# Optimization experiments

Measured on AMD Instinct MI355X. Metric: run time of the kernel, lower is better.

Reference implementation:

```python
import jax, jax.numpy as jnp
import numpy as np

NUM_BITS = 4
BLOCK = 64
OUT_F, IN_F = 4096, 4096
RANK = 16


def _uniform_table():
    # BlockQuantizer.create_uniform_map(symmetric=False, num_bits=4)
    return jnp.linspace(-1.0, 1.0, 2 ** NUM_BITS).astype(jnp.float32)


def _dequantize(qweight, weight_max):
    """Unpack 4-bit codes (2 per byte), lookup codebook, apply per-64 block scale.
    qweight: [OUT*IN/2, 1] int32 in [0,256); weight_max: [OUT*IN/64, 1] float32.
    Returns [OUT_F, IN_F] float32."""
    table = _uniform_table()
    q = qweight[:, 0]
    idx_lo = q & 15          # packed at shift 0
    idx_hi = (q >> 4) & 15   # packed at shift 4
    w = jnp.stack([table[idx_lo], table[idx_hi]], axis=-1)  # [N/2, 2]
    w = w.reshape(-1, BLOCK) * weight_max                   # per-block scale
    return w.reshape(OUT_F, IN_F)


def setup_inputs() -> dict:
    key = jax.random.key(0)
    k1, k2, k3, k4, k5, k6 = jax.random.split(key, 6)
    x = jax.random.normal(k1, (4, 2048, IN_F), dtype=jnp.float32)
    qweight = jax.random.randint(k2, (OUT_F * IN_F // 2, 1), 0, 256, dtype=jnp.int32)
    weight_max = jax.random.uniform(k3, (OUT_F * IN_F // BLOCK, 1), dtype=jnp.float32,
                                    minval=0.01, maxval=1.0)
    lora_A = jax.random.normal(k4, (RANK, IN_F), dtype=jnp.float32) * 0.02
    lora_B = jax.random.normal(k5, (OUT_F, RANK), dtype=jnp.float32) * 0.02
    bias = jax.random.normal(k6, (OUT_F,), dtype=jnp.float32) * 0.02
    return {"x": x, "qweight": qweight, "weight_max": weight_max,
            "lora_A": lora_A, "lora_B": lora_B, "bias": bias}


def reference(x, qweight, weight_max, lora_A, lora_B, bias):
    # Dequantize block-quantized base weight, then linear + LoRA correction.
    W = _dequantize(qweight, weight_max)                     # [out, in]
    y = jnp.einsum('bsi,oi->bso', x, W) + bias               # base linear
    a = jnp.einsum('bsi,ri->bsr', x, lora_A)                 # lora_A(x)
    y = y + jnp.einsum('bsr,or->bso', a, lora_B)             # + lora_B(.)
    return y
```

## Files before the change

### kernel.cpp

```cpp
#include <hip/hip_runtime.h>
#include <hip/hip_bf16.h>
#include <stdint.h>

typedef __bf16 bf16_t;
typedef bf16_t bf16x8 __attribute__((ext_vector_type(8)));
typedef float f32x4 __attribute__((ext_vector_type(4)));

#define IN_F 4096
#define OUT_F 4096
#define M_ROWS 8192
#define RANK 16

__global__ __launch_bounds__(256)
void dequant_lora_kernel(const int* __restrict__ qw, const float* __restrict__ wmax,
                         const float* __restrict__ lA, const float* __restrict__ lB,
                         bf16_t* __restrict__ Wp) {
  const int tid = blockIdx.x * 256 + threadIdx.x;
  const int f0 = tid * 8;
  const int o  = f0 >> 12;
  const int i0 = f0 & (IN_F - 1);
  const int4 q4 = *(const int4*)(qw + (f0 >> 1));
  const float scale = wmax[f0 >> 6];
  const float st = scale * (2.0f / 15.0f);

  float v[8];
  {
    const int q0 = q4.x, q1 = q4.y, q2 = q4.z, q3 = q4.w;
    v[0] = (float)(q0 & 15)        * st - scale;
    v[1] = (float)((q0 >> 4) & 15) * st - scale;
    v[2] = (float)(q1 & 15)        * st - scale;
    v[3] = (float)((q1 >> 4) & 15) * st - scale;
    v[4] = (float)(q2 & 15)        * st - scale;
    v[5] = (float)((q2 >> 4) & 15) * st - scale;
    v[6] = (float)(q3 & 15)        * st - scale;
    v[7] = (float)((q3 >> 4) & 15) * st - scale;
  }

  const float* Brow = lB + o * RANK;
#pragma unroll
  for (int r = 0; r < RANK; ++r) {
    const float br = Brow[r];
    const float4 a0 = *(const float4*)(lA + r * IN_F + i0);
    const float4 a1 = *(const float4*)(lA + r * IN_F + i0 + 4);
    v[0] += br * a0.x; v[1] += br * a0.y; v[2] += br * a0.z; v[3] += br * a0.w;
    v[4] += br * a1.x; v[5] += br * a1.y; v[6] += br * a1.z; v[7] += br * a1.w;
  }

  bf16x8 ov;
#pragma unroll
  for (int j = 0; j < 8; ++j) ov[j] = (bf16_t)v[j];
  *(bf16x8*)(Wp + (size_t)f0) = ov;
}

__global__ __launch_bounds__(256)
void f32_to_bf16_kernel(const float* __restrict__ x, bf16_t* __restrict__ xb) {
  const size_t tid = (size_t)blockIdx.x * 256 + threadIdx.x;
  const float4 a0 = *(const float4*)(x + tid * 8);
  const float4 a1 = *(const float4*)(x + tid * 8 + 4);
  bf16x8 o;
  o[0] = (bf16_t)a0.x; o[1] = (bf16_t)a0.y; o[2] = (bf16_t)a0.z; o[3] = (bf16_t)a0.w;
  o[4] = (bf16_t)a1.x; o[5] = (bf16_t)a1.y; o[6] = (bf16_t)a1.z; o[7] = (bf16_t)a1.w;
  *(bf16x8*)(xb + tid * 8) = o;
}

__device__ __forceinline__ void gld(const bf16_t* src, char* dst) {
  __builtin_amdgcn_global_load_lds((const __attribute__((address_space(1))) void*)src,
                                   (__attribute__((address_space(3))) void*)dst, 16, 0, 0);
}

#define BARRIER() __builtin_amdgcn_s_barrier()
#define SBAR()    __builtin_amdgcn_sched_barrier(0)
#define WAIT_VM(n) asm volatile("s_waitcnt vmcnt(" #n ")" ::: "memory")

#define LDA(buf, m, cb) (*(const bf16x8*)(ldsA + ((buf)*32768 + aRowB + (m)*2048 + (cb))))
#define LDB(buf, n, cb) (*(const bf16x8*)(ldsB + ((buf)*32768 + bRowB + (n)*2048 + (cb))))

#define STAGE_A4(kt, buf) do { \
  _Pragma("unroll") for (int g = 0; g < 4; ++g) \
    gld(Asrc + ((size_t)g*64*IN_F + (size_t)(kt)*64), ldsA + ((buf)*32768 + g*8192 + tid*16)); \
} while (0)
#define STAGE_B4(kt, buf) do { \
  _Pragma("unroll") for (int g = 0; g < 4; ++g) \
    gld(Bsrc + ((size_t)g*64*IN_F + (size_t)(kt)*64), ldsB + ((buf)*32768 + g*8192 + tid*16)); \
} while (0)

#define LOADA2(dst, m0, buf) do { \
  dst[0][0] = LDA(buf, m0,     cA0); dst[0][1] = LDA(buf, m0,     cA1); \
  dst[1][0] = LDA(buf, (m0)+1, cA0); dst[1][1] = LDA(buf, (m0)+1, cA1); \
} while (0)

#define PREFETCH12(buf, BFN) do { \
  LOADA2(aF0, 0, buf); \
  _Pragma("unroll") for (int n = 0; n < 4; ++n) { \
    BFN[n][0] = LDB(buf, n, cA0); BFN[n][1] = LDB(buf, n, cA1); } \
} while (0)

#define MFMA_Q(Q, AF, BF) do { \
  SBAR(); \
  __builtin_amdgcn_s_setprio(1); \
  _Pragma("unroll") for (int kh = 0; kh < 2; ++kh) \
  _Pragma("unroll") for (int mm = 0; mm < 2; ++mm) \
  _Pragma("unroll") for (int n = 0; n < 4; ++n) \
    acc[2*(Q)+mm][n] = __builtin_amdgcn_mfma_f32_16x16x32_bf16( \
        AF[mm][kh], BF[n][kh], acc[2*(Q)+mm][n], 0, 0, 0); \
  __builtin_amdgcn_s_setprio(0); \
} while (0)

#define TILE_BODY(CUR, BFC) do { \
  LOADA2(aF1, 2, CUR); MFMA_Q(0, aF0, BFC); \
  LOADA2(aF0, 4, CUR); MFMA_Q(1, aF1, BFC); \
  LOADA2(aF1, 6, CUR); MFMA_Q(2, aF0, BFC); \
  MFMA_Q(3, aF1, BFC); \
} while (0)

#define TILE_END(CUR, tv, BFN) do { \
  SBAR(); BARRIER(); \
  if ((tv) < 62) { STAGE_A4((tv) + 2, CUR); STAGE_B4((tv) + 2, CUR); \
                   SBAR(); WAIT_VM(8); } \
  else           { WAIT_VM(0); } \
  SBAR(); BARRIER(); SBAR(); \
  PREFETCH12((CUR) ^ 1, BFN); \
} while (0)

__global__ __launch_bounds__(512, 2)
void gemm_pipe_kernel(const bf16_t* __restrict__ Xb, const bf16_t* __restrict__ Wp,
                      const float* __restrict__ bias, float* __restrict__ C) {
  __shared__ __align__(16) bf16_t As[2 * 16384];
  __shared__ __align__(16) bf16_t Bs[2 * 16384];
  char* ldsA = (char*)As;
  char* ldsB = (char*)Bs;

  const int tid  = threadIdx.x;
  const int lane = tid & 63;
  const int wave = tid >> 6;
  const int wr = wave >> 2;
  const int wc = wave & 3;
  const int r16 = lane & 15;
  const int kg  = lane >> 4;

  const int bid = blockIdx.x;
  const int bm = bid >> 4;
  const int bn = bid & 15;

  const int sr = tid >> 3;
  const int sc = ((tid & 7) ^ (sr & 7)) << 3;
  const bf16_t* Asrc = Xb + (size_t)(bm * 256 + sr) * IN_F + sc;
  const bf16_t* Bsrc = Wp + (size_t)(bn * 256 + sr) * IN_F + sc;

  const int aRowB = (wr * 128 + r16) * 128;
  const int bRowB = (wc * 64 + r16) * 128;
  const int cA0 = (kg * 16) ^ ((r16 & 7) << 4);
  const int cA1 = cA0 ^ 64;

  f32x4 acc[8][4] = {};
  bf16x8 aF0[2][2], aF1[2][2], bFe[4][2], bFo[4][2];

  STAGE_A4(0, 0); STAGE_B4(0, 0);
  STAGE_A4(1, 1); STAGE_B4(1, 1);
  WAIT_VM(8);
  BARRIER(); SBAR();
  PREFETCH12(0, bFe);

  for (int tt = 0; tt < 62; tt += 2) {
    TILE_BODY(0, bFe); TILE_END(0, tt,     bFo);
    TILE_BODY(1, bFo); TILE_END(1, tt + 1, bFe);
  }
  TILE_BODY(0, bFe); TILE_END(0, 62, bFo);
  TILE_BODY(1, bFo);

#pragma unroll
  for (int n = 0; n < 4; ++n) {
    const int col = bn * 256 + wc * 64 + n * 16 + r16;
    const float bv = bias[col];
#pragma unroll
    for (int m = 0; m < 8; ++m) {
      const int row0 = bm * 256 + wr * 128 + m * 16 + kg * 4;
#pragma unroll
      for (int r = 0; r < 4; ++r)
        C[(size_t)(row0 + r) * OUT_F + col] = acc[m][n][r] + bv;
    }
  }
}

extern "C" void kernel_launch(void* const* d_in, const int* in_sizes, int n_in,
                              void* d_out, int out_size, void* d_ws, size_t ws_size,
                              hipStream_t stream) {
  const float* x  = (const float*)d_in[0];
  const int*   qw = (const int*)d_in[1];
  const float* wm = (const float*)d_in[2];
  const float* lA = (const float*)d_in[3];
  const float* lB = (const float*)d_in[4];
  const float* bs = (const float*)d_in[5];
  float* out = (float*)d_out;

  bf16_t* Wp = (bf16_t*)d_ws;
  bf16_t* Xb = (bf16_t*)((char*)d_ws + (size_t)OUT_F * IN_F * 2);

  dequant_lora_kernel<<<OUT_F * IN_F / 8 / 256, 256, 0, stream>>>(qw, wm, lA, lB, Wp);
  f32_to_bf16_kernel<<<M_ROWS * IN_F / 8 / 256, 256, 0, stream>>>(x, Xb);
  gemm_pipe_kernel<<<(M_ROWS / 256) * (OUT_F / 256), 512, 0, stream>>>(Xb, Wp, bs, out);
}
```

Before: 344.0 us.

## Load GEMM A operand directly from global memory into registers, skip LDS staging

The GEMM kernel stops staging the X (A) tile through LDS. Each wave now loads its A fragments straight from global memory into registers a quarter-tile ahead, and only the weight (B) tile still goes through LDS double-buffering, which halves LDS footprint and barrier-coupled traffic. The dequant kernel is also remapped so each block covers an 8-row by 256-column tile, which gives better LoRA A reuse. The risk is that direct global A loads repeat across the four column waves and expose memory latency, which relies on L1/L2 hits and the prefetch distance.

```diff
diff --git a/kernel.cpp b/kernel.cpp
--- a/kernel.cpp
+++ b/kernel.cpp
@@ -15,10 +15,14 @@
 void dequant_lora_kernel(const int* __restrict__ qw, const float* __restrict__ wmax,
                          const float* __restrict__ lA, const float* __restrict__ lB,
                          bf16_t* __restrict__ Wp) {
-  const int tid = blockIdx.x * 256 + threadIdx.x;
-  const int f0 = tid * 8;
-  const int o  = f0 >> 12;
-  const int i0 = f0 & (IN_F - 1);
+  const int bid = blockIdx.x;
+  const int bo = bid >> 4;
+  const int bi = bid & 15;
+  const int t  = threadIdx.x;
+  const int o  = bo * 8 + (t >> 5);
+  const int i0 = bi * 256 + (t & 31) * 8;
+  const int f0 = o * IN_F + i0;
+
   const int4 q4 = *(const int4*)(qw + (f0 >> 1));
   const float scale = wmax[f0 >> 6];
   const float st = scale * (2.0f / 15.0f);
@@ -72,27 +76,26 @@
 #define SBAR()    __builtin_amdgcn_sched_barrier(0)
 #define WAIT_VM(n) asm volatile("s_waitcnt vmcnt(" #n ")" ::: "memory")
 
-#define LDA(buf, m, cb) (*(const bf16x8*)(ldsA + ((buf)*32768 + aRowB + (m)*2048 + (cb))))
-#define LDB(buf, n, cb) (*(const bf16x8*)(ldsB + ((buf)*32768 + bRowB + (n)*2048 + (cb))))
-
-#define STAGE_A4(kt, buf) do { \
+#define STAGE_B(kt, buf) do { \
   _Pragma("unroll") for (int g = 0; g < 4; ++g) \
-    gld(Asrc + ((size_t)g*64*IN_F + (size_t)(kt)*64), ldsA + ((buf)*32768 + g*8192 + tid*16)); \
-} while (0)
-#define STAGE_B4(kt, buf) do { \
-  _Pragma("unroll") for (int g = 0; g < 4; ++g) \
-    gld(Bsrc + ((size_t)g*64*IN_F + (size_t)(kt)*64), ldsB + ((buf)*32768 + g*8192 + tid*16)); \
-} while (0)
-
-#define LOADA2(dst, m0, buf) do { \
-  dst[0][0] = LDA(buf, m0,     cA0); dst[0][1] = LDA(buf, m0,     cA1); \
-  dst[1][0] = LDA(buf, (m0)+1, cA0); dst[1][1] = LDA(buf, (m0)+1, cA1); \
-} while (0)
-
-#define PREFETCH12(buf, BFN) do { \
-  LOADA2(aF0, 0, buf); \
+    gld(Bsrc + (size_t)g * 64 * IN_F + (size_t)(kt) * 64, \
+        ldsB + (buf) * 32768 + g * 8192 + tid * 16); \
+} while (0)
+
+#define LDB(buf, n, kh) \
+  (*(const bf16x8*)(ldsB + (buf)*32768 + bRowB + (n)*2048 + cB##kh))
+
+#define PREF_B(buf, BFN) do { \
   _Pragma("unroll") for (int n = 0; n < 4; ++n) { \
-    BFN[n][0] = LDB(buf, n, cA0); BFN[n][1] = LDB(buf, n, cA1); } \
+    BFN[n][0] = LDB(buf, n, 0); BFN[n][1] = LDB(buf, n, 1); } \
+} while (0)
+
+#define PREF_A(dst, Q, tv) do { \
+  const bf16_t* _ap = Abase + (size_t)((Q) * 32) * IN_F + (tv) * 64; \
+  dst[0][0] = *(const bf16x8*)(_ap); \
+  dst[0][1] = *(const bf16x8*)(_ap + 32); \
+  dst[1][0] = *(const bf16x8*)(_ap + (size_t)16 * IN_F); \
+  dst[1][1] = *(const bf16x8*)(_ap + (size_t)16 * IN_F + 32); \
 } while (0)
 
 #define MFMA_Q(Q, AF, BF) do { \
@@ -106,28 +109,26 @@
   __builtin_amdgcn_s_setprio(0); \
 } while (0)
 
-#define TILE_BODY(CUR, BFC) do { \
-  LOADA2(aF1, 2, CUR); MFMA_Q(0, aF0, BFC); \
-  LOADA2(aF0, 4, CUR); MFMA_Q(1, aF1, BFC); \
-  LOADA2(aF1, 6, CUR); MFMA_Q(2, aF0, BFC); \
-  MFMA_Q(3, aF1, BFC); \
+#define TILE_BODY(BFC, tv) do { \
+  PREF_A(aG1, 1, tv); MFMA_Q(0, aG0, BFC); \
+  PREF_A(aG0, 2, tv); MFMA_Q(1, aG1, BFC); \
+  PREF_A(aG1, 3, tv); MFMA_Q(2, aG0, BFC); \
+  MFMA_Q(3, aG1, BFC); \
 } while (0)
 
 #define TILE_END(CUR, tv, BFN) do { \
   SBAR(); BARRIER(); \
-  if ((tv) < 62) { STAGE_A4((tv) + 2, CUR); STAGE_B4((tv) + 2, CUR); \
-                   SBAR(); WAIT_VM(8); } \
+  if ((tv) < 62) { STAGE_B((tv) + 2, CUR); SBAR(); WAIT_VM(4); } \
   else           { WAIT_VM(0); } \
   SBAR(); BARRIER(); SBAR(); \
-  PREFETCH12((CUR) ^ 1, BFN); \
+  PREF_A(aG0, 0, (tv) + 1); \
+  PREF_B((CUR) ^ 1, BFN); \
 } while (0)
 
 __global__ __launch_bounds__(512, 2)
-void gemm_pipe_kernel(const bf16_t* __restrict__ Xb, const bf16_t* __restrict__ Wp,
-                      const float* __restrict__ bias, float* __restrict__ C) {
-  __shared__ __align__(16) bf16_t As[2 * 16384];
+void gemm_adirect_kernel(const bf16_t* __restrict__ Xb, const bf16_t* __restrict__ Wp,
+                         const float* __restrict__ bias, float* __restrict__ C) {
   __shared__ __align__(16) bf16_t Bs[2 * 16384];
-  char* ldsA = (char*)As;
   char* ldsB = (char*)Bs;
 
   const int tid  = threadIdx.x;
@@ -142,31 +143,31 @@
   const int bm = bid >> 4;
   const int bn = bid & 15;
 
-  const int sr = tid >> 3;
-  const int sc = ((tid & 7) ^ (sr & 7)) << 3;
-  const bf16_t* Asrc = Xb + (size_t)(bm * 256 + sr) * IN_F + sc;
-  const bf16_t* Bsrc = Wp + (size_t)(bn * 256 + sr) * IN_F + sc;
-
-  const int aRowB = (wr * 128 + r16) * 128;
+  const int sp = (tid & 7) ^ ((tid >> 3) & 7);
+  const bf16_t* Bsrc = Wp + (size_t)(bn * 256 + (tid >> 3)) * IN_F + sp * 8;
+
   const int bRowB = (wc * 64 + r16) * 128;
-  const int cA0 = (kg * 16) ^ ((r16 & 7) << 4);
-  const int cA1 = cA0 ^ 64;
+  const int cB0 = ((kg)     ^ (r16 & 7)) * 16;
+  const int cB1 = ((4 + kg) ^ (r16 & 7)) * 16;
+
+  const bf16_t* Abase = Xb + (size_t)(bm * 256 + wr * 128 + r16) * IN_F + kg * 8;
 
   f32x4 acc[8][4] = {};
-  bf16x8 aF0[2][2], aF1[2][2], bFe[4][2], bFo[4][2];
-
-  STAGE_A4(0, 0); STAGE_B4(0, 0);
-  STAGE_A4(1, 1); STAGE_B4(1, 1);
-  WAIT_VM(8);
+  bf16x8 aG0[2][2], aG1[2][2], bFe[4][2], bFo[4][2];
+
+  STAGE_B(0, 0);
+  STAGE_B(1, 1);
+  WAIT_VM(4);
   BARRIER(); SBAR();
-  PREFETCH12(0, bFe);
+  PREF_A(aG0, 0, 0);
+  PREF_B(0, bFe);
 
   for (int tt = 0; tt < 62; tt += 2) {
-    TILE_BODY(0, bFe); TILE_END(0, tt,     bFo);
-    TILE_BODY(1, bFo); TILE_END(1, tt + 1, bFe);
-  }
-  TILE_BODY(0, bFe); TILE_END(0, 62, bFo);
-  TILE_BODY(1, bFo);
+    TILE_BODY(bFe, tt);     TILE_END(0, tt,     bFo);
+    TILE_BODY(bFo, tt + 1); TILE_END(1, tt + 1, bFe);
+  }
+  TILE_BODY(bFe, 62); TILE_END(0, 62, bFo);
+  TILE_BODY(bFo, 63);
 
 #pragma unroll
   for (int n = 0; n < 4; ++n) {
@@ -196,7 +197,7 @@
   bf16_t* Wp = (bf16_t*)d_ws;
   bf16_t* Xb = (bf16_t*)((char*)d_ws + (size_t)OUT_F * IN_F * 2);
 
-  dequant_lora_kernel<<<OUT_F * IN_F / 8 / 256, 256, 0, stream>>>(qw, wm, lA, lB, Wp);
+  dequant_lora_kernel<<<8192, 256, 0, stream>>>(qw, wm, lA, lB, Wp);
   f32_to_bf16_kernel<<<M_ROWS * IN_F / 8 / 256, 256, 0, stream>>>(x, Xb);
-  gemm_pipe_kernel<<<(M_ROWS / 256) * (OUT_F / 256), 512, 0, stream>>>(Xb, Wp, bs, out);
-}
+  gemm_adirect_kernel<<<(M_ROWS / 256) * (OUT_F / 256), 512, 0, stream>>>(Xb, Wp, bs, out);
+}
```

Result: slower. 630.1 us (+83.1%).
